# Kernel tuning notes

Measured on AMD Instinct MI355X. Metric: run time of the kernel, lower is better.

Reference implementation:

```python
import jax, jax.numpy as jnp
import numpy as np

N_NODES = 10000
N_EDGES = 320000
NODE_DIM = 128
EDGE_DIM = 16
HIDDEN = 256
OUT = 8
N_GRAPHS = 64
BN_EPS = 1e-5


def setup_inputs() -> dict:
    key = jax.random.key(0)
    ks = jax.random.split(key, 32)
    s = 0.1  # weight scale for sane numerics
    inp = {
        "x": jax.random.normal(ks[0], (N_NODES, NODE_DIM), jnp.float32),
        "edge_index": jax.random.randint(ks[1], (2, N_EDGES), 0, N_NODES, jnp.int32),
        "edge_attr": jax.random.normal(ks[2], (N_EDGES, EDGE_DIM), jnp.float32),
        "batch": jnp.sort(jax.random.randint(ks[3], (N_NODES,), 0, N_GRAPHS, jnp.int32)),
        "Wl1": s * jax.random.normal(ks[4], (NODE_DIM, HIDDEN), jnp.float32),
        "Wr1": s * jax.random.normal(ks[5], (NODE_DIM, HIDDEN), jnp.float32),
        "We1": s * jax.random.normal(ks[6], (EDGE_DIM, HIDDEN), jnp.float32),
        "bl1": s * jax.random.normal(ks[7], (HIDDEN,), jnp.float32),
        "br1": s * jax.random.normal(ks[8], (HIDDEN,), jnp.float32),
        "att1": s * jax.random.normal(ks[9], (HIDDEN,), jnp.float32),
        "b1": s * jax.random.normal(ks[10], (HIDDEN,), jnp.float32),
        "Wls": s * jax.random.normal(ks[11], (4, HIDDEN, HIDDEN), jnp.float32),
        "Wrs": s * jax.random.normal(ks[12], (4, HIDDEN, HIDDEN), jnp.float32),
        "Wes": s * jax.random.normal(ks[13], (4, EDGE_DIM, HIDDEN), jnp.float32),
        "bls": s * jax.random.normal(ks[14], (4, HIDDEN), jnp.float32),
        "brs": s * jax.random.normal(ks[15], (4, HIDDEN), jnp.float32),
        "atts": s * jax.random.normal(ks[16], (4, HIDDEN), jnp.float32),
        "bs": s * jax.random.normal(ks[17], (4, HIDDEN), jnp.float32),
        "bn_gamma": 0.5 + jax.random.uniform(ks[18], (5, HIDDEN), jnp.float32),
        "bn_beta": s * jax.random.normal(ks[19], (5, HIDDEN), jnp.float32),
        "bn_mean": s * jax.random.normal(ks[20], (5, HIDDEN), jnp.float32),
        "bn_var": 0.5 + jax.random.uniform(ks[21], (5, HIDDEN), jnp.float32),
        "lin1_w": s * jax.random.normal(ks[22], (HIDDEN, OUT), jnp.float32),
        "lin1_b": s * jax.random.normal(ks[23], (OUT,), jnp.float32),
        "lin2_w": s * jax.random.normal(ks[24], (HIDDEN, OUT), jnp.float32),
        "lin2_b": s * jax.random.normal(ks[25], (OUT,), jnp.float32),
    }
    return inp


def gatv2_conv(x, src, dst, edge_attr, Wl, Wr, We, bl, br, att, b, n_nodes):
    # GATv2 (heads=1): score_ij = att . leaky_relu(Wl x_j + Wr x_i + We e_ij, 0.2)
    xl = x @ Wl + bl                      # [N,H] source transform
    xr = x @ Wr + br                      # [N,H] target transform
    e = edge_attr @ We                    # [E,H]
    m = jax.nn.leaky_relu(xl[src] + xr[dst] + e, 0.2)  # [E,H]
    s = m @ att                           # [E]
    smax = jax.ops.segment_max(s, dst, num_segments=n_nodes)
    ex = jnp.exp(s - smax[dst])
    den = jax.ops.segment_sum(ex, dst, num_segments=n_nodes)
    alpha = ex / den[dst]                 # segment softmax over incoming edges
    out = jax.ops.segment_sum(alpha[:, None] * xl[src], dst, num_segments=n_nodes)
    return out + b


def batchnorm_eval(x, gamma, beta, mean, var):
    return (x - mean) * jax.lax.rsqrt(var + BN_EPS) * gamma + beta


def reference(x, edge_index, edge_attr, batch,
              Wl1, Wr1, We1, bl1, br1, att1, b1,
              Wls, Wrs, Wes, bls, brs, atts, bs,
              bn_gamma, bn_beta, bn_mean, bn_var,
              lin1_w, lin1_b, lin2_w, lin2_b):
    n = x.shape[0]
    src, dst = edge_index[0], edge_index[1]
    h = gatv2_conv(x, src, dst, edge_attr, Wl1, Wr1, We1, bl1, br1, att1, b1, n)
    h = batchnorm_eval(h, bn_gamma[0], bn_beta[0], bn_mean[0], bn_var[0])
    h = jax.nn.leaky_relu(h, 0.01)
    for i in range(4):  # convs 2..5 (fixed small layer count)
        h = gatv2_conv(h, src, dst, edge_attr, Wls[i], Wrs[i], Wes[i],
                       bls[i], brs[i], atts[i], bs[i], n)
        h = batchnorm_eval(h, bn_gamma[i + 1], bn_beta[i + 1], bn_mean[i + 1], bn_var[i + 1])
        h = jax.nn.relu(h) if i == 3 else jax.nn.leaky_relu(h, 0.01)
    # global mean pool per graph
    sums = jax.ops.segment_sum(h, batch, num_segments=N_GRAPHS)
    cnts = jax.ops.segment_sum(jnp.ones((n,), h.dtype), batch, num_segments=N_GRAPHS)
    g = sums / jnp.maximum(cnts, 1.0)[:, None]
    # dropout disabled (eval mode)
    pred1 = g @ lin1_w + lin1_b
    pred2 = g @ lin2_w + lin2_b
    return pred1, pred2
```

## Files before the change

kernel.cpp:

```cpp
#include <hip/hip_runtime.h>

#define N_NODES 10000
#define N_EDGES 320000
#define NODE_DIM 128
#define EDGE_DIM 16
#define HIDDEN 256
#define N_OUT 8
#define N_GRAPHS 64
#define LOG2E 1.4426950408889634f

typedef float f32x4 __attribute__((ext_vector_type(4)));
typedef short bf16x8 __attribute__((ext_vector_type(8)));
typedef _Float16 half2_t __attribute__((ext_vector_type(2)));

__device__ __forceinline__ unsigned short f2bf(float f) {
  unsigned int u = __float_as_uint(f);
  unsigned int r = (u + 0x7fff + ((u >> 16) & 1)) >> 16;
  return (unsigned short)r;
}

__device__ __forceinline__ unsigned int packh2(float a, float b) {
  half2_t h;
  h.x = (_Float16)a;
  h.y = (_Float16)b;
  return __builtin_bit_cast(unsigned int, h);
}

__global__ void hist_kernel(const int* __restrict__ dst, int* __restrict__ counts, int E) {
  int e = blockIdx.x * blockDim.x + threadIdx.x;
  if (e < E) atomicAdd(&counts[dst[e]], 1);
}

__global__ void scan_kernel(const int* __restrict__ counts, int* __restrict__ offs,
                            int* __restrict__ cursor, int n) {
  __shared__ int part[256];
  int t = threadIdx.x;
  const int chunk = (n + 255) / 256;
  int base = t * chunk;
  int s = 0;
  for (int j = 0; j < chunk; ++j) { int i = base + j; if (i < n) s += counts[i]; }
  part[t] = s;
  __syncthreads();
  for (int off = 1; off < 256; off <<= 1) {
    int v = (t >= off) ? part[t - off] : 0;
    __syncthreads();
    part[t] += v;
    __syncthreads();
  }
  int run = (t == 0) ? 0 : part[t - 1];
  for (int j = 0; j < chunk; ++j) {
    int i = base + j;
    if (i < n) { offs[i] = run; cursor[i] = run; run += counts[i]; }
  }
  if (t == 255) offs[n] = run;
}

__global__ void scatter_kernel(const int* __restrict__ ei, const float* __restrict__ eattr,
                               int* __restrict__ cursor, int* __restrict__ csr_src,
                               unsigned int* __restrict__ attr16, int E) {
  int e = blockIdx.x * blockDim.x + threadIdx.x;
  if (e >= E) return;
  int s = ei[e];
  int d = ei[E + e];
  int slot = atomicAdd(&cursor[d], 1);
  csr_src[slot] = s;
  const float4* in = (const float4*)(eattr + (size_t)e * 16);
  float4 v0 = in[0], v1 = in[1], v2 = in[2], v3 = in[3];
  uint4 o0, o1;
  o0.x = packh2(v0.x, v0.y); o0.y = packh2(v0.z, v0.w);
  o0.z = packh2(v1.x, v1.y); o0.w = packh2(v1.z, v1.w);
  o1.x = packh2(v2.x, v2.y); o1.y = packh2(v2.z, v2.w);
  o1.z = packh2(v3.x, v3.y); o1.w = packh2(v3.z, v3.w);
  uint4* outp = (uint4*)(attr16 + (size_t)slot * 8);
  outp[0] = o0; outp[1] = o1;
}

__global__ void cvt_w_all(const float* __restrict__ Wl1, const float* __restrict__ Wr1,
                          const float* __restrict__ Wls, const float* __restrict__ Wrs,
                          unsigned short* __restrict__ WTall) {
  const int layer = blockIdx.y;
  const int K = (layer == 0) ? NODE_DIM : HIDDEN;
  int idx = blockIdx.x * 256 + threadIdx.x;
  if (idx >= 512 * K) return;
  int n = idx / K, k = idx - n * K;
  const float* Wl = (layer == 0) ? Wl1 : Wls + (size_t)(layer - 1) * HIDDEN * HIDDEN;
  const float* Wr = (layer == 0) ? Wr1 : Wrs + (size_t)(layer - 1) * HIDDEN * HIDDEN;
  float v = (n < 256) ? Wl[(size_t)k * 256 + n] : Wr[(size_t)k * 256 + (n - 256)];
  WTall[(size_t)layer * 512 * 256 + idx] = f2bf(v);
}

__global__ void cvt_wep(const float* __restrict__ We1, const float* __restrict__ Wes,
                        unsigned int* __restrict__ WePall) {
  int idx = blockIdx.x * 256 + threadIdx.x;
  if (idx >= 5 * 8 * 256) return;
  int layer = idx >> 11;
  int rem = idx & 2047;
  int dp = rem >> 8, col = rem & 255;
  const float* W = (layer == 0) ? We1 : Wes + (size_t)(layer - 1) * EDGE_DIM * HIDDEN;
  WePall[idx] = packh2(W[(2 * dp) * HIDDEN + col], W[(2 * dp + 1) * HIDDEN + col]);
}

__global__ void cvt_x(const float* __restrict__ X, unsigned short* __restrict__ XB, int total4) {
  int idx = blockIdx.x * 256 + threadIdx.x;
  if (idx >= total4) return;
  float4 v = *(const float4*)(X + (size_t)idx * 4);
  ushort4 o;
  o.x = f2bf(v.x); o.y = f2bf(v.y); o.z = f2bf(v.z); o.w = f2bf(v.w);
  *(ushort4*)(XB + (size_t)idx * 4) = o;
}

__global__ __launch_bounds__(256) void gemm_mfma(
    const unsigned short* __restrict__ A,
    const unsigned short* __restrict__ WT,
    const float* __restrict__ bl, const float* __restrict__ br,
    float* __restrict__ C, int M, int K) {
  __shared__ unsigned short Atile[64 * 256];
  const int t = threadIdx.x;
  const int wv = t >> 6;
  const int l = t & 63;
  const int bm = blockIdx.x * 64;
  const int bn = blockIdx.y * 128;
  const int CPR = K >> 3;
  const int nchunks = 64 * CPR;

  for (int p = t; p < nchunks; p += 256) {
    const int r = p / CPR;
    const int c = p - r * CPR;
    int gr = bm + r; if (gr >= M) gr = M - 1;
    const uint4 v = *(const uint4*)(A + (size_t)gr * K + c * 8);
    const int eff = c ^ (r & 7);
    *(uint4*)((char*)Atile + ((size_t)r * CPR + eff) * 16) = v;
  }
  __syncthreads();

  const int col0 = bn + wv * 32 + (l & 15);
  const int col1 = col0 + 16;
  const int kg = l >> 4;
  f32x4 acc[4][2];
#pragma unroll
  for (int mt = 0; mt < 4; ++mt) {
    acc[mt][0] = (f32x4){0.f, 0.f, 0.f, 0.f};
    acc[mt][1] = (f32x4){0.f, 0.f, 0.f, 0.f};
  }
  const int steps = K >> 5;
  for (int ks = 0; ks < steps; ++ks) {
    const bf16x8 bf0 = *(const bf16x8*)(WT + (size_t)col0 * K + ks * 32 + kg * 8);
    const bf16x8 bf1 = *(const bf16x8*)(WT + (size_t)col1 * K + ks * 32 + kg * 8);
#pragma unroll
    for (int mt = 0; mt < 4; ++mt) {
      const int row = mt * 16 + (l & 15);
      const int eff = (ks * 4 + kg) ^ (row & 7);
      const bf16x8 af = *(const bf16x8*)((const char*)Atile + ((size_t)row * CPR + eff) * 16);
      acc[mt][0] = __builtin_amdgcn_mfma_f32_16x16x32_bf16(af, bf0, acc[mt][0], 0, 0, 0);
      acc[mt][1] = __builtin_amdgcn_mfma_f32_16x16x32_bf16(af, bf1, acc[mt][1], 0, 0, 0);
    }
  }
  const float bias0 = (col0 < 256) ? bl[col0] : br[col0 - 256];
  const float bias1 = (col1 < 256) ? bl[col1] : br[col1 - 256];
#pragma unroll
  for (int mt = 0; mt < 4; ++mt) {
#pragma unroll
    for (int j = 0; j < 4; ++j) {
      int row = bm + mt * 16 + (l >> 4) * 4 + j;
      if (row < M) {
        C[(size_t)row * 512 + col0] = acc[mt][0][j] + bias0;
        C[(size_t)row * 512 + col1] = acc[mt][1][j] + bias1;
      }
    }
  }
}

__global__ __launch_bounds__(256, 4) void edge_gat(
    const float* __restrict__ xlr,
    const int* __restrict__ offs, const int* __restrict__ csr_src,
    const unsigned int* __restrict__ attr16,
    const unsigned int* __restrict__ WeP, const float* __restrict__ att,
    const float* __restrict__ bconv,
    const float* __restrict__ gamma, const float* __restrict__ beta,
    const float* __restrict__ mean, const float* __restrict__ var,
    float* __restrict__ hout, unsigned short* __restrict__ hbf, int relu_last) {
  const int t = threadIdx.x;
  const int w = t >> 6;
  const int l = t & 63;
  const int h4 = l << 2;
  const int iu = __builtin_amdgcn_readfirstlane(blockIdx.x * 4 + w);

  float4 att4 = *(const float4*)(att + h4);
  att4.x *= LOG2E; att4.y *= LOG2E; att4.z *= LOG2E; att4.w *= LOG2E;
  const float4 xr4 = *(const float4*)(xlr + (size_t)iu * 512 + HIDDEN + h4);

  const int rs = __builtin_amdgcn_readfirstlane(offs[iu]);
  const int re = __builtin_amdgcn_readfirstlane(offs[iu + 1]);

  float mrun = -1e30f, den = 0.f;
  float4 acc = make_float4(0.f, 0.f, 0.f, 0.f);

  for (int e = rs; e < re; e += 4) {
    const int e0 = e;
    const int e1 = (e + 1 < re) ? e + 1 : e;
    const int e2 = (e + 2 < re) ? e + 2 : e;
    const int e3 = (e + 3 < re) ? e + 3 : e;
    const int s0 = __builtin_amdgcn_readfirstlane(csr_src[e0]);
    const int s1 = __builtin_amdgcn_readfirstlane(csr_src[e1]);
    const int s2 = __builtin_amdgcn_readfirstlane(csr_src[e2]);
    const int s3 = __builtin_amdgcn_readfirstlane(csr_src[e3]);
    const float4 xl0 = *(const float4*)(xlr + (size_t)s0 * 512 + h4);
    const float4 xl1 = *(const float4*)(xlr + (size_t)s1 * 512 + h4);
    const float4 xl2 = *(const float4*)(xlr + (size_t)s2 * 512 + h4);
    const float4 xl3 = *(const float4*)(xlr + (size_t)s3 * 512 + h4);

    float z0x = 0.f, z0y = 0.f, z0z = 0.f, z0w = 0.f;
    float z1x = 0.f, z1y = 0.f, z1z = 0.f, z1w = 0.f;
    float z2x = 0.f, z2y = 0.f, z2z = 0.f, z2w = 0.f;
    float z3x = 0.f, z3y = 0.f, z3z = 0.f, z3w = 0.f;

#pragma unroll
    for (int dp = 0; dp < 8; ++dp) {
      const uint4 wb = *(const uint4*)(WeP + dp * HIDDEN + h4);
      const half2_t wx = __builtin_bit_cast(half2_t, wb.x);
      const half2_t wy = __builtin_bit_cast(half2_t, wb.y);
      const half2_t wz = __builtin_bit_cast(half2_t, wb.z);
      const half2_t ww = __builtin_bit_cast(half2_t, wb.w);
      const half2_t a0 = __builtin_bit_cast(half2_t, attr16[(size_t)e0 * 8 + dp]);
      const half2_t a1 = __builtin_bit_cast(half2_t, attr16[(size_t)e1 * 8 + dp]);
      const half2_t a2 = __builtin_bit_cast(half2_t, attr16[(size_t)e2 * 8 + dp]);
      const half2_t a3 = __builtin_bit_cast(half2_t, attr16[(size_t)e3 * 8 + dp]);
      z0x = __builtin_amdgcn_fdot2(a0, wx, z0x, false);
      z0y = __builtin_amdgcn_fdot2(a0, wy, z0y, false);
      z0z = __builtin_amdgcn_fdot2(a0, wz, z0z, false);
      z0w = __builtin_amdgcn_fdot2(a0, ww, z0w, false);
      z1x = __builtin_amdgcn_fdot2(a1, wx, z1x, false);
      z1y = __builtin_amdgcn_fdot2(a1, wy, z1y, false);
      z1z = __builtin_amdgcn_fdot2(a1, wz, z1z, false);
      z1w = __builtin_amdgcn_fdot2(a1, ww, z1w, false);
      z2x = __builtin_amdgcn_fdot2(a2, wx, z2x, false);
      z2y = __builtin_amdgcn_fdot2(a2, wy, z2y, false);
      z2z = __builtin_amdgcn_fdot2(a2, wz, z2z, false);
      z2w = __builtin_amdgcn_fdot2(a2, ww, z2w, false);
      z3x = __builtin_amdgcn_fdot2(a3, wx, z3x, false);
      z3y = __builtin_amdgcn_fdot2(a3, wy, z3y, false);
      z3z = __builtin_amdgcn_fdot2(a3, wz, z3z, false);
      z3w = __builtin_amdgcn_fdot2(a3, ww, z3w, false);
    }

    float p0, p1, p2, p3;
    {
      float zx, zy, zz, zw;
      zx = z0x + xr4.x + xl0.x; zy = z0y + xr4.y + xl0.y;
      zz = z0z + xr4.z + xl0.z; zw = z0w + xr4.w + xl0.w;
      zx = fmaxf(zx, 0.2f * zx); zy = fmaxf(zy, 0.2f * zy);
      zz = fmaxf(zz, 0.2f * zz); zw = fmaxf(zw, 0.2f * zw);
      p0 = att4.x * zx; p0 = fmaf(att4.y, zy, p0); p0 = fmaf(att4.z, zz, p0); p0 = fmaf(att4.w, zw, p0);
      zx = z1x + xr4.x + xl1.x; zy = z1y + xr4.y + xl1.y;
      zz = z1z + xr4.z + xl1.z; zw = z1w + xr4.w + xl1.w;
      zx = fmaxf(zx, 0.2f * zx); zy = fmaxf(zy, 0.2f * zy);
      zz = fmaxf(zz, 0.2f * zz); zw = fmaxf(zw, 0.2f * zw);
      p1 = att4.x * zx; p1 = fmaf(att4.y, zy, p1); p1 = fmaf(att4.z, zz, p1); p1 = fmaf(att4.w, zw, p1);
      zx = z2x + xr4.x + xl2.x; zy = z2y + xr4.y + xl2.y;
      zz = z2z + xr4.z + xl2.z; zw = z2w + xr4.w + xl2.w;
      zx = fmaxf(zx, 0.2f * zx); zy = fmaxf(zy, 0.2f * zy);
      zz = fmaxf(zz, 0.2f * zz); zw = fmaxf(zw, 0.2f * zw);
      p2 = att4.x * zx; p2 = fmaf(att4.y, zy, p2); p2 = fmaf(att4.z, zz, p2); p2 = fmaf(att4.w, zw, p2);
      zx = z3x + xr4.x + xl3.x; zy = z3y + xr4.y + xl3.y;
      zz = z3z + xr4.z + xl3.z; zw = z3w + xr4.w + xl3.w;
      zx = fmaxf(zx, 0.2f * zx); zy = fmaxf(zy, 0.2f * zy);
      zz = fmaxf(zz, 0.2f * zz); zw = fmaxf(zw, 0.2f * zw);
      p3 = att4.x * zx; p3 = fmaf(att4.y, zy, p3); p3 = fmaf(att4.z, zz, p3); p3 = fmaf(att4.w, zw, p3);
    }

#pragma unroll
    for (int off = 32; off > 0; off >>= 1) {
      p0 += __shfl_xor(p0, off, 64);
      p1 += __shfl_xor(p1, off, 64);
      p2 += __shfl_xor(p2, off, 64);
      p3 += __shfl_xor(p3, off, 64);
    }
    if (e + 1 >= re) p1 = -1e30f;
    if (e + 2 >= re) p2 = -1e30f;
    if (e + 3 >= re) p3 = -1e30f;

    const float bmx = fmaxf(fmaxf(p0, p1), fmaxf(p2, p3));
    const float nm = fmaxf(mrun, bmx);
    const float sc = exp2f(mrun - nm);
    const float w0 = exp2f(p0 - nm);
    const float w1 = exp2f(p1 - nm);
    const float w2 = exp2f(p2 - nm);
    const float w3 = exp2f(p3 - nm);
    den = fmaf(den, sc, (w0 + w1) + (w2 + w3));
    float tx = w0 * xl0.x; tx = fmaf(w1, xl1.x, tx); tx = fmaf(w2, xl2.x, tx); tx = fmaf(w3, xl3.x, tx);
    float ty = w0 * xl0.y; ty = fmaf(w1, xl1.y, ty); ty = fmaf(w2, xl2.y, ty); ty = fmaf(w3, xl3.y, ty);
    float tz = w0 * xl0.z; tz = fmaf(w1, xl1.z, tz); tz = fmaf(w2, xl2.z, tz); tz = fmaf(w3, xl3.z, tz);
    float tw = w0 * xl0.w; tw = fmaf(w1, xl1.w, tw); tw = fmaf(w2, xl2.w, tw); tw = fmaf(w3, xl3.w, tw);
    acc.x = fmaf(acc.x, sc, tx);
    acc.y = fmaf(acc.y, sc, ty);
    acc.z = fmaf(acc.z, sc, tz);
    acc.w = fmaf(acc.w, sc, tw);
    mrun = nm;
  }

  const float inv = (den > 0.f) ? __frcp_rn(den) : 0.f;
  const float4 bc4 = *(const float4*)(bconv + h4);
  const float4 g4 = *(const float4*)(gamma + h4);
  const float4 b4 = *(const float4*)(beta + h4);
  const float4 m4 = *(const float4*)(mean + h4);
  const float4 v4 = *(const float4*)(var + h4);
  float o[4] = {acc.x, acc.y, acc.z, acc.w};
  const float bc[4] = {bc4.x, bc4.y, bc4.z, bc4.w};
  const float gm[4] = {g4.x, g4.y, g4.z, g4.w};
  const float bt[4] = {b4.x, b4.y, b4.z, b4.w};
  const float mn[4] = {m4.x, m4.y, m4.z, m4.w};
  const float vr[4] = {v4.x, v4.y, v4.z, v4.w};
  float res[4];
#pragma unroll
  for (int j = 0; j < 4; ++j) {
    float y = fmaf(o[j], inv, bc[j]);
    y = (y - mn[j]) * rsqrtf(vr[j] + 1e-5f) * gm[j] + bt[j];
    res[j] = relu_last ? fmaxf(y, 0.f) : fmaxf(y, 0.01f * y);
  }
  if (relu_last) {
    float4 rf = {res[0], res[1], res[2], res[3]};
    *(float4*)(hout + (size_t)iu * HIDDEN + h4) = rf;
  }
  ushort4 rb;
  rb.x = f2bf(res[0]); rb.y = f2bf(res[1]); rb.z = f2bf(res[2]); rb.w = f2bf(res[3]);
  *(ushort4*)(hbf + (size_t)iu * HIDDEN + h4) = rb;
}

__device__ __forceinline__ int lbound(const int* a, int n, int v) {
  int lo = 0, hi = n;
  while (lo < hi) { int m = (lo + hi) >> 1; if (a[m] < v) lo = m + 1; else hi = m; }
  return lo;
}

__global__ void pool_kernel(const float* __restrict__ h, const int* __restrict__ batch,
                            float* __restrict__ g) {
  const int gi = blockIdx.x;
  const int t = threadIdx.x;
  int s = lbound(batch, N_NODES, gi);
  int e = lbound(batch, N_NODES, gi + 1);
  float sum = 0.f;
  for (int i = s; i < e; ++i) sum += h[(size_t)i * HIDDEN + t];
  float c = (float)(e - s);
  g[gi * HIDDEN + t] = sum / fmaxf(c, 1.f);
}

__global__ void head_kernel(const float* __restrict__ g,
                            const float* __restrict__ w1, const float* __restrict__ b1,
                            const float* __restrict__ w2, const float* __restrict__ b2,
                            float* __restrict__ out) {
  int idx = blockIdx.x * 256 + threadIdx.x;
  if (idx >= N_GRAPHS * N_OUT * 2) return;
  int which = idx >> 9;
  int rem = idx & 511;
  int row = rem >> 3, col = rem & 7;
  const float* w = which ? w2 : w1;
  float s = which ? b2[col] : b1[col];
  for (int k = 0; k < HIDDEN; ++k) s = fmaf(g[row * HIDDEN + k], w[k * N_OUT + col], s);
  out[idx] = s;
}

extern "C" void kernel_launch(void* const* d_in, const int* in_sizes, int n_in,
                              void* d_out, int out_size, void* d_ws, size_t ws_size,
                              hipStream_t stream) {
  const float* x     = (const float*)d_in[0];
  const int*   ei    = (const int*)d_in[1];
  const float* eattr = (const float*)d_in[2];
  const int*   batch = (const int*)d_in[3];
  const float* Wl1   = (const float*)d_in[4];
  const float* Wr1   = (const float*)d_in[5];
  const float* We1   = (const float*)d_in[6];
  const float* bl1   = (const float*)d_in[7];
  const float* br1   = (const float*)d_in[8];
  const float* att1  = (const float*)d_in[9];
  const float* b1    = (const float*)d_in[10];
  const float* Wls   = (const float*)d_in[11];
  const float* Wrs   = (const float*)d_in[12];
  const float* Wes   = (const float*)d_in[13];
  const float* bls   = (const float*)d_in[14];
  const float* brs   = (const float*)d_in[15];
  const float* atts  = (const float*)d_in[16];
  const float* bs    = (const float*)d_in[17];
  const float* bng   = (const float*)d_in[18];
  const float* bnb   = (const float*)d_in[19];
  const float* bnm   = (const float*)d_in[20];
  const float* bnv   = (const float*)d_in[21];
  const float* l1w   = (const float*)d_in[22];
  const float* l1b   = (const float*)d_in[23];
  const float* l2w   = (const float*)d_in[24];
  const float* l2b   = (const float*)d_in[25];
  float* out = (float*)d_out;

  char* ws = (char*)d_ws;
  auto alloc = [&](size_t bytes) {
    char* p = ws;
    ws += (bytes + 255) & ~(size_t)255;
    return p;
  };
  int*   counts   = (int*)alloc((size_t)N_NODES * 4);
  int*   offs     = (int*)alloc((size_t)(N_NODES + 1) * 4);
  int*   cursor   = (int*)alloc((size_t)N_NODES * 4);
  int*   csr_src  = (int*)alloc((size_t)N_EDGES * 4);
  unsigned int* attr16 = (unsigned int*)alloc((size_t)N_EDGES * 8 * 4);
  unsigned int* WePall = (unsigned int*)alloc((size_t)5 * 8 * 256 * 4);
  float* xlr      = (float*)alloc((size_t)N_NODES * 512 * 4);
  float* hF       = (float*)alloc((size_t)N_NODES * 256 * 4);
  unsigned short* hbf0 = (unsigned short*)alloc((size_t)N_NODES * 256 * 2);
  unsigned short* hbf1 = (unsigned short*)alloc((size_t)N_NODES * 256 * 2);
  unsigned short* xbf  = (unsigned short*)alloc((size_t)N_NODES * NODE_DIM * 2);
  unsigned short* WTall = (unsigned short*)alloc((size_t)5 * 512 * 256 * 2);
  float* g        = (float*)alloc((size_t)N_GRAPHS * 256 * 4);

  hipMemsetAsync(counts, 0, (size_t)N_NODES * 4, stream);
  hist_kernel<<<(N_EDGES + 255) / 256, 256, 0, stream>>>(ei + N_EDGES, counts, N_EDGES);
  scan_kernel<<<1, 256, 0, stream>>>(counts, offs, cursor, N_NODES);
  scatter_kernel<<<(N_EDGES + 255) / 256, 256, 0, stream>>>(ei, eattr, cursor, csr_src,
                                                            attr16, N_EDGES);
  cvt_x<<<(N_NODES * NODE_DIM / 4 + 255) / 256, 256, 0, stream>>>(x, xbf,
                                                                  N_NODES * NODE_DIM / 4);
  {
    dim3 wgrid(512, 5);
    cvt_w_all<<<wgrid, 256, 0, stream>>>(Wl1, Wr1, Wls, Wrs, WTall);
  }
  cvt_wep<<<(5 * 8 * 256 + 255) / 256, 256, 0, stream>>>(We1, Wes, WePall);

  for (int layer = 0; layer < 5; ++layer) {
    int K = (layer == 0) ? NODE_DIM : HIDDEN;
    const float* bl = (layer == 0) ? bl1 : bls + (layer - 1) * HIDDEN;
    const float* br = (layer == 0) ? br1 : brs + (layer - 1) * HIDDEN;
    const float* at = (layer == 0) ? att1 : atts + (layer - 1) * HIDDEN;
    const float* bc = (layer == 0) ? b1 : bs + (layer - 1) * HIDDEN;
    const unsigned short* Abf = (layer == 0) ? xbf : ((layer & 1) ? hbf0 : hbf1);
    unsigned short* hbf_out = (layer & 1) ? hbf1 : hbf0;
    const unsigned short* WT = WTall + (size_t)layer * 512 * 256;
    const unsigned int* WeP = WePall + (size_t)layer * 8 * 256;

    dim3 ggrid((N_NODES + 63) / 64, 4);
    gemm_mfma<<<ggrid, 256, 0, stream>>>(Abf, WT, bl, br, xlr, N_NODES, K);
    edge_gat<<<N_NODES / 4, 256, 0, stream>>>(xlr, offs, csr_src, attr16, WeP, at, bc,
                                              bng + layer * HIDDEN, bnb + layer * HIDDEN,
                                              bnm + layer * HIDDEN, bnv + layer * HIDDEN,
                                              hF, hbf_out, (layer == 4) ? 1 : 0);
  }
  pool_kernel<<<N_GRAPHS, 256, 0, stream>>>(hF, batch, g);
  head_kernel<<<4, 256, 0, stream>>>(g, l1w, l1b, l2w, l2b, out);
}
```

Baseline: 517.4 us.

## Store projected node features in bf16 and enlarge GEMM row tile

The GEMM now writes the left/right projections xlr as bf16 instead of fp32, and the edge kernel gathers and widens them back to fp32. This halves the bytes moved by the per-edge random gathers of source-node features, which dominate the edge kernel. The GEMM row tile also doubles from 64 to 128 rows, giving more B-operand reuse but fewer blocks and larger LDS and register use. The right-node term is now folded into the initial accumulator, and bf16 storage loses some precision in the attention logits.

```diff
diff --git a/kernel.cpp b/kernel.cpp
--- a/kernel.cpp
+++ b/kernel.cpp
@@ -17,6 +17,10 @@
   unsigned int u = __float_as_uint(f);
   unsigned int r = (u + 0x7fff + ((u >> 16) & 1)) >> 16;
   return (unsigned short)r;
+}
+
+__device__ __forceinline__ float bf2f(unsigned short u) {
+  return __uint_as_float((unsigned int)u << 16);
 }
 
 __device__ __forceinline__ unsigned int packh2(float a, float b) {
@@ -113,15 +117,15 @@
     const unsigned short* __restrict__ A,
     const unsigned short* __restrict__ WT,
     const float* __restrict__ bl, const float* __restrict__ br,
-    float* __restrict__ C, int M, int K) {
-  __shared__ unsigned short Atile[64 * 256];
+    unsigned short* __restrict__ C, int M, int K) {
+  __shared__ unsigned short Atile[128 * 256];
   const int t = threadIdx.x;
   const int wv = t >> 6;
   const int l = t & 63;
-  const int bm = blockIdx.x * 64;
+  const int bm = blockIdx.x * 128;
   const int bn = blockIdx.y * 128;
   const int CPR = K >> 3;
-  const int nchunks = 64 * CPR;
+  const int nchunks = 128 * CPR;
 
   for (int p = t; p < nchunks; p += 256) {
     const int r = p / CPR;
@@ -136,9 +140,9 @@
   const int col0 = bn + wv * 32 + (l & 15);
   const int col1 = col0 + 16;
   const int kg = l >> 4;
-  f32x4 acc[4][2];
-#pragma unroll
-  for (int mt = 0; mt < 4; ++mt) {
+  f32x4 acc[8][2];
+#pragma unroll
+  for (int mt = 0; mt < 8; ++mt) {
     acc[mt][0] = (f32x4){0.f, 0.f, 0.f, 0.f};
     acc[mt][1] = (f32x4){0.f, 0.f, 0.f, 0.f};
   }
@@ -147,7 +151,7 @@
     const bf16x8 bf0 = *(const bf16x8*)(WT + (size_t)col0 * K + ks * 32 + kg * 8);
     const bf16x8 bf1 = *(const bf16x8*)(WT + (size_t)col1 * K + ks * 32 + kg * 8);
 #pragma unroll
-    for (int mt = 0; mt < 4; ++mt) {
+    for (int mt = 0; mt < 8; ++mt) {
       const int row = mt * 16 + (l & 15);
       const int eff = (ks * 4 + kg) ^ (row & 7);
       const bf16x8 af = *(const bf16x8*)((const char*)Atile + ((size_t)row * CPR + eff) * 16);
@@ -158,20 +162,20 @@
   const float bias0 = (col0 < 256) ? bl[col0] : br[col0 - 256];
   const float bias1 = (col1 < 256) ? bl[col1] : br[col1 - 256];
 #pragma unroll
-  for (int mt = 0; mt < 4; ++mt) {
+  for (int mt = 0; mt < 8; ++mt) {
 #pragma unroll
     for (int j = 0; j < 4; ++j) {
       int row = bm + mt * 16 + (l >> 4) * 4 + j;
       if (row < M) {
-        C[(size_t)row * 512 + col0] = acc[mt][0][j] + bias0;
-        C[(size_t)row * 512 + col1] = acc[mt][1][j] + bias1;
+        C[(size_t)row * 512 + col0] = f2bf(acc[mt][0][j] + bias0);
+        C[(size_t)row * 512 + col1] = f2bf(acc[mt][1][j] + bias1);
       }
     }
   }
 }
 
 __global__ __launch_bounds__(256, 4) void edge_gat(
-    const float* __restrict__ xlr,
+    const unsigned short* __restrict__ xlr,
     const int* __restrict__ offs, const int* __restrict__ csr_src,
     const unsigned int* __restrict__ attr16,
     const unsigned int* __restrict__ WeP, const float* __restrict__ att,
@@ -187,7 +191,8 @@
 
   float4 att4 = *(const float4*)(att + h4);
   att4.x *= LOG2E; att4.y *= LOG2E; att4.z *= LOG2E; att4.w *= LOG2E;
-  const float4 xr4 = *(const float4*)(xlr + (size_t)iu * 512 + HIDDEN + h4);
+  const ushort4 xru = *(const ushort4*)(xlr + (size_t)iu * 512 + HIDDEN + h4);
+  const float4 xr4 = {bf2f(xru.x), bf2f(xru.y), bf2f(xru.z), bf2f(xru.w)};
 
   const int rs = __builtin_amdgcn_readfirstlane(offs[iu]);
   const int re = __builtin_amdgcn_readfirstlane(offs[iu + 1]);
@@ -204,15 +209,19 @@
     const int s1 = __builtin_amdgcn_readfirstlane(csr_src[e1]);
     const int s2 = __builtin_amdgcn_readfirstlane(csr_src[e2]);
     const int s3 = __builtin_amdgcn_readfirstlane(csr_src[e3]);
-    const float4 xl0 = *(const float4*)(xlr + (size_t)s0 * 512 + h4);
-    const float4 xl1 = *(const float4*)(xlr + (size_t)s1 * 512 + h4);
-    const float4 xl2 = *(const float4*)(xlr + (size_t)s2 * 512 + h4);
-    const float4 xl3 = *(const float4*)(xlr + (size_t)s3 * 512 + h4);
-
-    float z0x = 0.f, z0y = 0.f, z0z = 0.f, z0w = 0.f;
-    float z1x = 0.f, z1y = 0.f, z1z = 0.f, z1w = 0.f;
-    float z2x = 0.f, z2y = 0.f, z2z = 0.f, z2w = 0.f;
-    float z3x = 0.f, z3y = 0.f, z3z = 0.f, z3w = 0.f;
+    const ushort4 xu0 = *(const ushort4*)(xlr + (size_t)s0 * 512 + h4);
+    const ushort4 xu1 = *(const ushort4*)(xlr + (size_t)s1 * 512 + h4);
+    const ushort4 xu2 = *(const ushort4*)(xlr + (size_t)s2 * 512 + h4);
+    const ushort4 xu3 = *(const ushort4*)(xlr + (size_t)s3 * 512 + h4);
+    const float4 xl0 = {bf2f(xu0.x), bf2f(xu0.y), bf2f(xu0.z), bf2f(xu0.w)};
+    const float4 xl1 = {bf2f(xu1.x), bf2f(xu1.y), bf2f(xu1.z), bf2f(xu1.w)};
+    const float4 xl2 = {bf2f(xu2.x), bf2f(xu2.y), bf2f(xu2.z), bf2f(xu2.w)};
+    const float4 xl3 = {bf2f(xu3.x), bf2f(xu3.y), bf2f(xu3.z), bf2f(xu3.w)};
+
+    float z0x = xr4.x, z0y = xr4.y, z0z = xr4.z, z0w = xr4.w;
+    float z1x = xr4.x, z1y = xr4.y, z1z = xr4.z, z1w = xr4.w;
+    float z2x = xr4.x, z2y = xr4.y, z2z = xr4.z, z2w = xr4.w;
+    float z3x = xr4.x, z3y = xr4.y, z3z = xr4.z, z3w = xr4.w;
 
 #pragma unroll
     for (int dp = 0; dp < 8; ++dp) {
@@ -246,23 +255,19 @@
     float p0, p1, p2, p3;
     {
       float zx, zy, zz, zw;
-      zx = z0x + xr4.x + xl0.x; zy = z0y + xr4.y + xl0.y;
-      zz = z0z + xr4.z + xl0.z; zw = z0w + xr4.w + xl0.w;
+      zx = z0x + xl0.x; zy = z0y + xl0.y; zz = z0z + xl0.z; zw = z0w + xl0.w;
       zx = fmaxf(zx, 0.2f * zx); zy = fmaxf(zy, 0.2f * zy);
       zz = fmaxf(zz, 0.2f * zz); zw = fmaxf(zw, 0.2f * zw);
       p0 = att4.x * zx; p0 = fmaf(att4.y, zy, p0); p0 = fmaf(att4.z, zz, p0); p0 = fmaf(att4.w, zw, p0);
-      zx = z1x + xr4.x + xl1.x; zy = z1y + xr4.y + xl1.y;
-      zz = z1z + xr4.z + xl1.z; zw = z1w + xr4.w + xl1.w;
+      zx = z1x + xl1.x; zy = z1y + xl1.y; zz = z1z + xl1.z; zw = z1w + xl1.w;
       zx = fmaxf(zx, 0.2f * zx); zy = fmaxf(zy, 0.2f * zy);
       zz = fmaxf(zz, 0.2f * zz); zw = fmaxf(zw, 0.2f * zw);
       p1 = att4.x * zx; p1 = fmaf(att4.y, zy, p1); p1 = fmaf(att4.z, zz, p1); p1 = fmaf(att4.w, zw, p1);
-      zx = z2x + xr4.x + xl2.x; zy = z2y + xr4.y + xl2.y;
-      zz = z2z + xr4.z + xl2.z; zw = z2w + xr4.w + xl2.w;
+      zx = z2x + xl2.x; zy = z2y + xl2.y; zz = z2z + xl2.z; zw = z2w + xl2.w;
       zx = fmaxf(zx, 0.2f * zx); zy = fmaxf(zy, 0.2f * zy);
       zz = fmaxf(zz, 0.2f * zz); zw = fmaxf(zw, 0.2f * zw);
       p2 = att4.x * zx; p2 = fmaf(att4.y, zy, p2); p2 = fmaf(att4.z, zz, p2); p2 = fmaf(att4.w, zw, p2);
-      zx = z3x + xr4.x + xl3.x; zy = z3y + xr4.y + xl3.y;
-      zz = z3z + xr4.z + xl3.z; zw = z3w + xr4.w + xl3.w;
+      zx = z3x + xl3.x; zy = z3y + xl3.y; zz = z3z + xl3.z; zw = z3w + xl3.w;
       zx = fmaxf(zx, 0.2f * zx); zy = fmaxf(zy, 0.2f * zy);
       zz = fmaxf(zz, 0.2f * zz); zw = fmaxf(zw, 0.2f * zw);
       p3 = att4.x * zx; p3 = fmaf(att4.y, zy, p3); p3 = fmaf(att4.z, zz, p3); p3 = fmaf(att4.w, zw, p3);
@@ -402,7 +407,7 @@
   int*   csr_src  = (int*)alloc((size_t)N_EDGES * 4);
   unsigned int* attr16 = (unsigned int*)alloc((size_t)N_EDGES * 8 * 4);
   unsigned int* WePall = (unsigned int*)alloc((size_t)5 * 8 * 256 * 4);
-  float* xlr      = (float*)alloc((size_t)N_NODES * 512 * 4);
+  unsigned short* xlr  = (unsigned short*)alloc((size_t)N_NODES * 512 * 2);
   float* hF       = (float*)alloc((size_t)N_NODES * 256 * 4);
   unsigned short* hbf0 = (unsigned short*)alloc((size_t)N_NODES * 256 * 2);
   unsigned short* hbf1 = (unsigned short*)alloc((size_t)N_NODES * 256 * 2);
@@ -434,7 +439,7 @@
     const unsigned short* WT = WTall + (size_t)layer * 512 * 256;
     const unsigned int* WeP = WePall + (size_t)layer * 8 * 256;
 
-    dim3 ggrid((N_NODES + 63) / 64, 4);
+    dim3 ggrid((N_NODES + 127) / 128, 4);
     gemm_mfma<<<ggrid, 256, 0, stream>>>(Abf, WT, bl, br, xlr, N_NODES, K);
     edge_gat<<<N_NODES / 4, 256, 0, stream>>>(xlr, offs, csr_src, attr16, WeP, at, bc,
                                               bng + layer * HIDDEN, bnb + layer * HIDDEN,
```

New measurement: 527.1 us. No clear change (+1.9%).
